# Optimization experiments

Hardware: AMD Instinct MI355X
Metric: run time of the kernel (lower is better)

Reference implementation:

```python
import jax, jax.numpy as jnp
import numpy as np

KSIZE = 15
SIGMA = 3.0
PAD = KSIZE // 2


def _gauss_kernel2d():
    g = jnp.arange(KSIZE, dtype=jnp.float32) - KSIZE // 2
    g = jnp.exp(-(g ** 2) / (2.0 * SIGMA * SIGMA))
    g = g / g.sum()
    return g[:, None] * g[None, :]  # [15,15]


def _depthwise_blur(x, k2):
    # x: [B,C,H,W]; 15x15 Gaussian applied per channel (matches per-channel F.conv2d loop)
    C = x.shape[1]
    kernel = jnp.broadcast_to(k2[None, None], (C, 1, KSIZE, KSIZE))
    return jax.lax.conv_general_dilated(
        x, kernel, window_strides=(1, 1), padding=[(PAD, PAD), (PAD, PAD)],
        feature_group_count=C, dimension_numbers=("NCHW", "OIHW", "NCHW"))


def setup_inputs() -> dict:
    key = jax.random.key(0)
    B, C, H, W = 4, 3, 1024, 1024
    x = jax.random.uniform(key, (B, C, H, W), dtype=jnp.float32)
    f32 = lambda v: jnp.asarray(v, dtype=jnp.float32)
    return {
        "x": x,
        "gains": jnp.array([1.1, 1.0, 0.9], dtype=jnp.float32),
        "gamma": f32(0.9),
        "shadow_boost": f32(0.1),
        "highlight_reduce": f32(0.1),
        "brightness": f32(0.05),
        "contrast": f32(1.1),
        "enhance_amount": f32(0.8),
        "softness": f32(0.6),
        "intensity": f32(0.3),
        "rotation": f32(30.0),
        "hardness": f32(2.0),
    }


def reference(x, gains, gamma, shadow_boost, highlight_reduce, brightness,
              contrast, enhance_amount, softness, intensity, rotation, hardness):
    B, C, H, W = x.shape
    k2 = _gauss_kernel2d()

    # WhiteBalanceAdjustment
    x = x * gains.reshape(1, C, 1, 1)
    # ToneCurveAdjustment
    x = jnp.power(x, gamma)
    # ShadowHighlightEnhancement
    hi = jax.nn.sigmoid((x - 0.5) * 10.0)
    x = jnp.clip(x + shadow_boost * (1.0 - hi) - highlight_reduce * hi, 0.0, 1.0)
    # GlobalBrightnessContrastAdjustment
    x = jnp.clip(contrast * (x - 0.5) + 0.5 + brightness, 0.0, 1.0)
    # LocalContrastEnhancement
    local_mean = _depthwise_blur(x, k2)
    x = x + enhance_amount * (x - local_mean)
    # SoftnessFilter
    blurred = _depthwise_blur(x, k2)
    x = softness * blurred + (1.0 - softness) * x
    # GradientNDAdjustment
    ys = jnp.linspace(-1.0, 1.0, H, dtype=jnp.float32)
    xs = jnp.linspace(-1.0, 1.0, W, dtype=jnp.float32)
    grid_y, grid_x = jnp.meshgrid(ys, xs, indexing="ij")
    theta = rotation * (np.pi / 180.0)
    grid_rot = grid_x * jnp.cos(theta) + grid_y * jnp.sin(theta)
    mask = jax.nn.sigmoid(-hardness * grid_rot)[None, None]  # [1,1,H,W]
    x = jnp.clip(x * (1.0 - intensity * mask), 0.0, 1.0)

    return jnp.clip(x, 0.0, 1.0)
```

## Files before the change

### kernel.cpp

```cpp
#include <hip/hip_runtime.h>
#include <math.h>

#define HH 1024
#define WW 1024
#define NPLANES 12
#define PLANE (HH * WW)
#define NTOT (NPLANES * PLANE)

#define TW 64
#define TH 64
#define HR 78
#define PITCH 68

struct W15 { float w[15]; };

__device__ inline float4 ld4z(const float* __restrict__ row, int x) {
    if (x >= 0 && x + 3 < WW) return *(const float4*)(row + x);
    float4 r; float* p = (float*)&r;
#pragma unroll
    for (int j = 0; j < 4; ++j) { int xx = x + j; p[j] = (xx >= 0 && xx < WW) ? row[xx] : 0.0f; }
    return r;
}

__device__ inline float chain1(float t, float gain, float gamma, float sb,
                               float hr, float br, float ct) {
    t = t * gain;
    t = __builtin_amdgcn_exp2f(gamma * __log2f(t));
    float hi = __fdividef(1.0f, 1.0f + __expf((0.5f - t) * 10.0f));
    t = t + sb * (1.0f - hi) - hr * hi;
    t = fminf(fmaxf(t, 0.0f), 1.0f);
    t = ct * (t - 0.5f) + 0.5f + br;
    return fminf(fmaxf(t, 0.0f), 1.0f);
}

__device__ inline float4 hdot4(const float f[20], const W15& wk) {
    float4 o; float* po = (float*)&o;
#pragma unroll
    for (int j = 0; j < 4; ++j) {
        float a = 0.0f, b = 0.0f;
#pragma unroll
        for (int k = 0; k < 8; ++k)  a += wk.w[k] * f[j + 1 + k];
#pragma unroll
        for (int k = 8; k < 15; ++k) b += wk.w[k] * f[j + 1 + k];
        po[j] = a + b;
    }
    return o;
}

__global__ __launch_bounds__(256) void k_point(
    const float4* __restrict__ x, float4* __restrict__ o,
    const float* __restrict__ gains,
    const float* __restrict__ pg, const float* __restrict__ psb,
    const float* __restrict__ phr, const float* __restrict__ pbr,
    const float* __restrict__ pct)
{
    int i = blockIdx.x * blockDim.x + threadIdx.x;
    if (i >= NTOT / 4) return;
    int c = ((i * 4) / PLANE) % 3;
    float gain = gains[c];
    float gamma = *pg, sb = *psb, hr = *phr, br = *pbr, ct = *pct;

    float4 v = x[i];
    float* pv = (float*)&v;
#pragma unroll
    for (int j = 0; j < 4; ++j)
        pv[j] = chain1(pv[j], gain, gamma, sb, hr, br, ct);
    o[i] = v;
}

__device__ inline void hblur_stage(const float* __restrict__ plane, float* __restrict__ hbl,
                                   int x0, int y0, int tid, bool edge, const W15& wk)
{
    const int cx = (tid & 15) * 4;
    const int r0 = tid >> 4;
    if (!edge) {
#pragma unroll
        for (int it = 0; it < 5; ++it) {
            int r = r0 + 16 * it;
            if (r < HR) {
                const float* rp = plane + (size_t)(y0 - 7 + r) * WW + (x0 + cx - 8);
                float f[20];
                *(float4*)&f[0]  = *(const float4*)(rp);
                *(float4*)&f[4]  = *(const float4*)(rp + 4);
                *(float4*)&f[8]  = *(const float4*)(rp + 8);
                *(float4*)&f[12] = *(const float4*)(rp + 12);
                *(float4*)&f[16] = *(const float4*)(rp + 16);
                *(float4*)&hbl[r * PITCH + cx] = hdot4(f, wk);
            }
        }
    } else {
        for (int it = 0; it < 5; ++it) {
            int r = r0 + 16 * it;
            if (r < HR) {
                int gy = y0 - 7 + r;
                float4 o;
                if (gy >= 0 && gy < HH) {
                    const float* row = plane + (size_t)gy * WW;
                    int xb = x0 + cx - 8;
                    float f[20];
                    *(float4*)&f[0]  = ld4z(row, xb);
                    *(float4*)&f[4]  = ld4z(row, xb + 4);
                    *(float4*)&f[8]  = ld4z(row, xb + 8);
                    *(float4*)&f[12] = ld4z(row, xb + 12);
                    *(float4*)&f[16] = ld4z(row, xb + 16);
                    o = hdot4(f, wk);
                } else {
                    o = make_float4(0.0f, 0.0f, 0.0f, 0.0f);
                }
                *(float4*)&hbl[r * PITCH + cx] = o;
            }
        }
    }
}

__global__ __launch_bounds__(256) void k_blur_lce(
    const float* __restrict__ t0, float* __restrict__ x2,
    const float* __restrict__ penh, W15 wk)
{
    __shared__ float hbl[HR * PITCH];
    const int p   = blockIdx.z;
    const int x0  = blockIdx.x * TW;
    const int y0  = blockIdx.y * TH;
    const int tid = threadIdx.x;
    const float* plane = t0 + (size_t)p * PLANE;
    const bool edge = (blockIdx.x == 0) || (blockIdx.x == WW / TW - 1) ||
                      (blockIdx.y == 0) || (blockIdx.y == HH / TH - 1);

    hblur_stage(plane, hbl, x0, y0, tid, edge, wk);
    __syncthreads();

    const int tx  = tid & 63;
    const int ty  = tid >> 6;
    const int ly0 = ty * 16;
    const int gx  = x0 + tx;
    const float e = *penh;

    float win[15];
#pragma unroll
    for (int k = 0; k < 15; ++k) win[k] = hbl[(ly0 + k) * PITCH + tx];

    float* dstP = x2 + (size_t)p * PLANE;
#pragma unroll
    for (int j = 0; j < 16; ++j) {
        int y = y0 + ly0 + j;
        float a = 0.0f, b = 0.0f;
#pragma unroll
        for (int k = 0; k < 8; ++k)  a += wk.w[k] * win[k];
#pragma unroll
        for (int k = 8; k < 15; ++k) b += wk.w[k] * win[k];
        float lm = a + b;
        float c = plane[(size_t)y * WW + gx];
        dstP[(size_t)y * WW + gx] = (1.0f + e) * c - e * lm;
#pragma unroll
        for (int k = 0; k < 14; ++k) win[k] = win[k + 1];
        win[14] = hbl[(ly0 + j + 15) * PITCH + tx];
    }
}

__global__ __launch_bounds__(256) void k_blur_final(
    const float* __restrict__ x2, float* __restrict__ dst,
    const float* __restrict__ psoft, const float* __restrict__ pint,
    const float* __restrict__ prot, const float* __restrict__ phard, W15 wk)
{
    __shared__ float hbl[HR * PITCH];
    const int p   = blockIdx.z;
    const int x0  = blockIdx.x * TW;
    const int y0  = blockIdx.y * TH;
    const int tid = threadIdx.x;
    const float* plane = x2 + (size_t)p * PLANE;
    const bool edge = (blockIdx.x == 0) || (blockIdx.x == WW / TW - 1) ||
                      (blockIdx.y == 0) || (blockIdx.y == HH / TH - 1);

    hblur_stage(plane, hbl, x0, y0, tid, edge, wk);
    __syncthreads();

    const int tx  = tid & 63;
    const int ty  = tid >> 6;
    const int ly0 = ty * 16;
    const int gx  = x0 + tx;

    const float s     = *psoft;
    const float inten = *pint;
    const float hard  = *phard;
    const float theta = (*prot) * 0.017453292519943295f;
    const float cth = __cosf(theta), sth = __sinf(theta);
    const float base = (-1.0f + 2.0f * (float)gx * (1.0f / (float)(WW - 1))) * cth;

    float win[15];
#pragma unroll
    for (int k = 0; k < 15; ++k) win[k] = hbl[(ly0 + k) * PITCH + tx];

    float* dstP = dst + (size_t)p * PLANE;
#pragma unroll
    for (int j = 0; j < 16; ++j) {
        int y = y0 + ly0 + j;
        float a = 0.0f, b = 0.0f;
#pragma unroll
        for (int k = 0; k < 8; ++k)  a += wk.w[k] * win[k];
#pragma unroll
        for (int k = 8; k < 15; ++k) b += wk.w[k] * win[k];
        float bl = a + b;
        float c = plane[(size_t)y * WW + gx];
        float v = s * bl + (1.0f - s) * c;
        float gyf = -1.0f + 2.0f * (float)y * (1.0f / (float)(HH - 1));
        float mask = __fdividef(1.0f, 1.0f + __expf(hard * (base + gyf * sth)));
        v = v * (1.0f - inten * mask);
        v = fminf(fmaxf(v, 0.0f), 1.0f);
        dstP[(size_t)y * WW + gx] = v;
#pragma unroll
        for (int k = 0; k < 14; ++k) win[k] = win[k + 1];
        win[14] = hbl[(ly0 + j + 15) * PITCH + tx];
    }
}

extern "C" void kernel_launch(void* const* d_in, const int* in_sizes, int n_in,
                              void* d_out, int out_size, void* d_ws, size_t ws_size,
                              hipStream_t stream)
{
    const float* x       = (const float*)d_in[0];
    const float* gains   = (const float*)d_in[1];
    const float* p_gamma = (const float*)d_in[2];
    const float* p_sb    = (const float*)d_in[3];
    const float* p_hr    = (const float*)d_in[4];
    const float* p_br    = (const float*)d_in[5];
    const float* p_ct    = (const float*)d_in[6];
    const float* p_enh   = (const float*)d_in[7];
    const float* p_soft  = (const float*)d_in[8];
    const float* p_int   = (const float*)d_in[9];
    const float* p_rot   = (const float*)d_in[10];
    const float* p_hard  = (const float*)d_in[11];

    float* T0  = (float*)d_out;
    float* X2  = (float*)d_ws;
    float* OUT = (float*)d_out;

    W15 wk;
    {
        double g[15], sum = 0.0;
        for (int i = 0; i < 15; ++i) { double d = (double)(i - 7); g[i] = exp(-d * d / 18.0); sum += g[i]; }
        for (int i = 0; i < 15; ++i) wk.w[i] = (float)(g[i] / sum);
    }

    k_point<<<dim3(NTOT / 4 / 256), dim3(256), 0, stream>>>(
        (const float4*)x, (float4*)T0, gains, p_gamma, p_sb, p_hr, p_br, p_ct);

    dim3 grid(WW / TW, HH / TH, NPLANES);
    k_blur_lce<<<grid, dim3(256), 0, stream>>>(T0, X2, p_enh, wk);
    k_blur_final<<<grid, dim3(256), 0, stream>>>(X2, OUT, p_soft, p_int, p_rot, p_hard, wk);
}
```

Baseline: 190.2 us.

## Remap blur tiles per XCD, double-buffer row loads, and hoist center loads

Adds a block-index remap so each of the 8 XCDs handles a contiguous range of tiles (384 per XCD, grouped by plane). This keeps neighbouring tiles' halo rows in the same XCD's L2. The interior horizontal-blur stage double-buffers the 20-float row loads so the next row's global fetch is issued before the current row is computed. Both blur kernels now preload their 16 center pixels into registers before the vertical pass, so those global loads are not serialised inside the loop. The cost is more register pressure, and the remap hardcodes the grid size and the 8-XCD round-robin assumption.

Measured after the change: 186.8 us. No clear change (-1.8%).

```diff
diff --git a/kernel.cpp b/kernel.cpp
--- a/kernel.cpp
+++ b/kernel.cpp
@@ -33,7 +33,7 @@
     return fminf(fmaxf(t, 0.0f), 1.0f);
 }
 
-__device__ inline float4 hdot4(const float f[20], const W15& wk) {
+__device__ inline float4 hdot4(const float* f, const W15& wk) {
     float4 o; float* po = (float*)&o;
 #pragma unroll
     for (int j = 0; j < 4; ++j) {
@@ -68,25 +68,43 @@
     o[i] = v;
 }
 
+__device__ inline void tile_map(int& p, int& x0, int& y0, bool& edge) {
+    int L = (blockIdx.z * gridDim.y + blockIdx.y) * gridDim.x + blockIdx.x;
+    int xcd = L & 7;
+    int t   = L >> 3;
+    int g   = xcd * 384 + t;
+    p = g >> 8;
+    int w  = g & 255;
+    int ty = w >> 4, tx = w & 15;
+    x0 = tx * TW; y0 = ty * TH;
+    edge = (tx == 0) || (tx == 15) || (ty == 0) || (ty == 15);
+}
+
+__device__ inline void ldrow20(float* f, const float* rp) {
+    *(float4*)&f[0]  = *(const float4*)(rp);
+    *(float4*)&f[4]  = *(const float4*)(rp + 4);
+    *(float4*)&f[8]  = *(const float4*)(rp + 8);
+    *(float4*)&f[12] = *(const float4*)(rp + 12);
+    *(float4*)&f[16] = *(const float4*)(rp + 16);
+}
+
 __device__ inline void hblur_stage(const float* __restrict__ plane, float* __restrict__ hbl,
                                    int x0, int y0, int tid, bool edge, const W15& wk)
 {
     const int cx = (tid & 15) * 4;
     const int r0 = tid >> 4;
     if (!edge) {
+        const float* base = plane + (size_t)(y0 - 7) * WW + (x0 + cx - 8);
+        float f[2][20];
+        ldrow20(f[0], base + (size_t)r0 * WW);
 #pragma unroll
         for (int it = 0; it < 5; ++it) {
-            int r = r0 + 16 * it;
-            if (r < HR) {
-                const float* rp = plane + (size_t)(y0 - 7 + r) * WW + (x0 + cx - 8);
-                float f[20];
-                *(float4*)&f[0]  = *(const float4*)(rp);
-                *(float4*)&f[4]  = *(const float4*)(rp + 4);
-                *(float4*)&f[8]  = *(const float4*)(rp + 8);
-                *(float4*)&f[12] = *(const float4*)(rp + 12);
-                *(float4*)&f[16] = *(const float4*)(rp + 16);
-                *(float4*)&hbl[r * PITCH + cx] = hdot4(f, wk);
-            }
+            int r  = r0 + 16 * it;
+            int rn = r + 16;
+            if (it < 4 && rn < HR)
+                ldrow20(f[(it + 1) & 1], base + (size_t)rn * WW);
+            if (r < HR)
+                *(float4*)&hbl[r * PITCH + cx] = hdot4(f[it & 1], wk);
         }
     } else {
         for (int it = 0; it < 5; ++it) {
@@ -118,13 +136,10 @@
     const float* __restrict__ penh, W15 wk)
 {
     __shared__ float hbl[HR * PITCH];
-    const int p   = blockIdx.z;
-    const int x0  = blockIdx.x * TW;
-    const int y0  = blockIdx.y * TH;
+    int p, x0, y0; bool edge;
+    tile_map(p, x0, y0, edge);
     const int tid = threadIdx.x;
     const float* plane = t0 + (size_t)p * PLANE;
-    const bool edge = (blockIdx.x == 0) || (blockIdx.x == WW / TW - 1) ||
-                      (blockIdx.y == 0) || (blockIdx.y == HH / TH - 1);
 
     hblur_stage(plane, hbl, x0, y0, tid, edge, wk);
     __syncthreads();
@@ -135,6 +150,10 @@
     const int gx  = x0 + tx;
     const float e = *penh;
 
+    float cc[16];
+#pragma unroll
+    for (int j = 0; j < 16; ++j) cc[j] = plane[(size_t)(y0 + ly0 + j) * WW + gx];
+
     float win[15];
 #pragma unroll
     for (int k = 0; k < 15; ++k) win[k] = hbl[(ly0 + k) * PITCH + tx];
@@ -149,8 +168,7 @@
 #pragma unroll
         for (int k = 8; k < 15; ++k) b += wk.w[k] * win[k];
         float lm = a + b;
-        float c = plane[(size_t)y * WW + gx];
-        dstP[(size_t)y * WW + gx] = (1.0f + e) * c - e * lm;
+        dstP[(size_t)y * WW + gx] = (1.0f + e) * cc[j] - e * lm;
 #pragma unroll
         for (int k = 0; k < 14; ++k) win[k] = win[k + 1];
         win[14] = hbl[(ly0 + j + 15) * PITCH + tx];
@@ -163,13 +181,10 @@
     const float* __restrict__ prot, const float* __restrict__ phard, W15 wk)
 {
     __shared__ float hbl[HR * PITCH];
-    const int p   = blockIdx.z;
-    const int x0  = blockIdx.x * TW;
-    const int y0  = blockIdx.y * TH;
+    int p, x0, y0; bool edge;
+    tile_map(p, x0, y0, edge);
     const int tid = threadIdx.x;
     const float* plane = x2 + (size_t)p * PLANE;
-    const bool edge = (blockIdx.x == 0) || (blockIdx.x == WW / TW - 1) ||
-                      (blockIdx.y == 0) || (blockIdx.y == HH / TH - 1);
 
     hblur_stage(plane, hbl, x0, y0, tid, edge, wk);
     __syncthreads();
@@ -186,6 +201,10 @@
     const float cth = __cosf(theta), sth = __sinf(theta);
     const float base = (-1.0f + 2.0f * (float)gx * (1.0f / (float)(WW - 1))) * cth;
 
+    float cc[16];
+#pragma unroll
+    for (int j = 0; j < 16; ++j) cc[j] = plane[(size_t)(y0 + ly0 + j) * WW + gx];
+
     float win[15];
 #pragma unroll
     for (int k = 0; k < 15; ++k) win[k] = hbl[(ly0 + k) * PITCH + tx];
@@ -200,8 +219,7 @@
 #pragma unroll
         for (int k = 8; k < 15; ++k) b += wk.w[k] * win[k];
         float bl = a + b;
-        float c = plane[(size_t)y * WW + gx];
-        float v = s * bl + (1.0f - s) * c;
+        float v = s * bl + (1.0f - s) * cc[j];
         float gyf = -1.0f + 2.0f * (float)y * (1.0f / (float)(HH - 1));
         float mask = __fdividef(1.0f, 1.0f + __expf(hard * (base + gyf * sth)));
         v = v * (1.0f - inten * mask);
```
